# Kernel tuning notes

Measured on AMD Instinct MI355X. Metric: run time of the kernel, lower is better.

Reference implementation:

```python
import jax, jax.numpy as jnp
import numpy as np
import math

B, T, H = 2, 1024, 2048
NH, NKV, HD = 8, 2, 256
S = 4           # altup_num_inputs
FF = 8192       # intermediate_size
LR = 64         # laurel_rank
EPS = 1e-6
ROPE_THETA = 1e6


def _ln(x, w):
    # Gemma3nRMSNorm in this repo: fp32 mean-subtract then F.layer_norm (no bias)
    x32 = x.astype(jnp.float32)
    xc = x32 - x32.mean(-1, keepdims=True)
    var = (xc * xc).mean(-1, keepdims=True)
    return (xc * jax.lax.rsqrt(var + EPS) * w.astype(jnp.float32)).astype(x.dtype)


def _rotate_half(x):
    x1, x2 = jnp.split(x, 2, axis=-1)
    return jnp.concatenate((-x2, x1), axis=-1)


def _rope(x, cos, sin):  # x: [B,nh,T,hd]; cos/sin: [B,T,hd]
    return x * cos[:, None] + _rotate_half(x) * sin[:, None]


def setup_inputs() -> dict:
    key = jax.random.key(0)
    ks = jax.random.split(key, 24)

    def w(k, shape, scale=0.02):
        return jax.random.normal(k, shape, jnp.float32) * scale

    hidden_states = jax.random.normal(ks[0], (S, B, T, H), jnp.float32)

    # real rotary embeddings
    inv_freq = 1.0 / (ROPE_THETA ** (np.arange(0, HD, 2, dtype=np.float64) / HD))
    freqs = np.arange(T, dtype=np.float64)[:, None] * inv_freq[None, :]
    emb = np.concatenate([freqs, freqs], axis=-1)  # [T,HD]
    cos = jnp.broadcast_to(jnp.asarray(np.cos(emb), jnp.float32)[None], (B, T, HD))
    sin = jnp.broadcast_to(jnp.asarray(np.sin(emb), jnp.float32)[None], (B, T, HD))

    return {
        "hidden_states": hidden_states, "cos": cos, "sin": sin,
        "wq": w(ks[1], (NH * HD, H)), "wk": w(ks[2], (NKV * HD, H)),
        "wv": w(ks[3], (NKV * HD, H)), "wo": w(ks[4], (H, NH * HD)),
        "q_norm_w": jnp.ones((HD,), jnp.float32), "k_norm_w": jnp.ones((HD,), jnp.float32),
        "input_ln_w": jnp.ones((H,), jnp.float32), "post_attn_ln_w": jnp.ones((H,), jnp.float32),
        "pre_ffw_ln_w": jnp.ones((H,), jnp.float32), "post_ffw_ln_w": jnp.ones((H,), jnp.float32),
        "gate_w": w(ks[5], (FF, H)), "up_w": w(ks[6], (FF, H)), "down_w": w(ks[7], (H, FF)),
        "laurel_left_w": w(ks[8], (LR, H)), "laurel_right_w": w(ks[9], (H, LR)),
        "laurel_norm_w": jnp.ones((H,), jnp.float32),
        "router_norm_w": jnp.ones((H,), jnp.float32),
        "router_w": w(ks[10], (S, H)),
        "pred_coef_w": w(ks[11], (S * S, S)),
        "corr_coef_w": w(ks[12], (S, S)),
        "correct_output_scale": w(ks[13], (H,), 1.0),
    }


def reference(hidden_states, cos, sin, wq, wk, wv, wo, q_norm_w, k_norm_w,
              input_ln_w, post_attn_ln_w, pre_ffw_ln_w, post_ffw_ln_w,
              gate_w, up_w, down_w, laurel_left_w, laurel_right_w, laurel_norm_w,
              router_norm_w, router_w, pred_coef_w, corr_coef_w, correct_output_scale):
    def modalities_of(x):  # router: RMSNorm -> scale -> linear -> tanh
        r = _ln(x, router_norm_w) * (1.0 / H)
        return jnp.tanh((r @ router_w.T).astype(jnp.float32)).astype(x.dtype)

    # ---- AltUp predict ----
    m = modalities_of(hidden_states[0])                      # [B,T,S]
    coefs = (m @ pred_coef_w.T).reshape(B, T, S, S)          # raw [B,T,S_out,S_in]
    # torch: matmul(h.permute(1,2,3,0), coefs.permute(0,1,3,2)) => sum_s h[s]*raw[...,j,s]
    predictions = jnp.einsum('sbth,btjs->jbth', hidden_states, coefs) + hidden_states

    active = predictions[0]
    x_norm = _ln(active, input_ln_w)

    # ---- Laurel block ----
    lau = (x_norm @ laurel_left_w.T) @ laurel_right_w.T
    laurel_out = x_norm + _ln(lau, laurel_norm_w)

    # ---- Attention (GQA, q/k/v norms, rope, scale=1.0) ----
    q = _ln((x_norm @ wq.T).reshape(B, T, NH, HD), q_norm_w).transpose(0, 2, 1, 3)
    q = _rope(q, cos, sin)
    k = _ln((x_norm @ wk.T).reshape(B, T, NKV, HD), k_norm_w).transpose(0, 2, 1, 3)
    k = _rope(k, cos, sin)
    v = _ln((x_norm @ wv.T).reshape(B, T, NKV, HD), jnp.ones((HD,), jnp.float32))
    v = v.transpose(0, 2, 1, 3)
    rep = NH // NKV
    k = jnp.repeat(k, rep, axis=1)
    v = jnp.repeat(v, rep, axis=1)
    scores = jnp.einsum('bhqd,bhkd->bhqk', q, k)             # scaling = 1.0 in Gemma3n
    causal = jnp.tril(jnp.ones((T, T), bool))
    scores = jnp.where(causal, scores, jnp.finfo(jnp.float32).min)
    attn = jax.nn.softmax(scores.astype(jnp.float32), axis=-1).astype(q.dtype)
    out = jnp.einsum('bhqk,bhkd->bhqd', attn, v)
    out = out.transpose(0, 2, 1, 3).reshape(B, T, NH * HD) @ wo.T
    out = _ln(out, post_attn_ln_w)

    attn_gated = active + out
    attn_laurel = (attn_gated + laurel_out) * (1.0 / math.sqrt(2.0))

    # ---- MLP (gelu-tanh gated) ----
    h = _ln(attn_laurel, pre_ffw_ln_w)
    ffw = (jax.nn.gelu(h @ gate_w.T, approximate=True) * (h @ up_w.T)) @ down_w.T
    ffw = _ln(ffw, post_ffw_ln_w)
    activated = attn_laurel + ffw

    # ---- AltUp correct ----
    mc = modalities_of(activated)                            # [B,T,S]
    innovation = activated - predictions[0]                  # [B,T,H]
    ccoefs = (mc @ corr_coef_w.T) + 1.0                      # [B,T,S]
    corrected = innovation[None] * ccoefs.transpose(2, 0, 1)[..., None] + predictions

    # scale_corrected_output on the active stream (altup_correct_scale=True)
    first = (corrected[0] * correct_output_scale).astype(corrected.dtype)
    corrected = corrected.at[0].set(first)
    return corrected
```

## Files before the change

### kernel.cpp

```cpp
#include <hip/hip_runtime.h>
#include <hip/hip_bf16.h>
#include <math.h>

#define B_   2
#define T_   1024
#define H_   2048
#define NH_  8
#define NKV_ 2
#define HD_  256
#define S_   4
#define FF_  8192
#define LR_  64
#define ROWS_ (B_*T_)
#define EPS_ 1e-6f

typedef __attribute__((ext_vector_type(8))) __bf16 bf16x8;
typedef __attribute__((ext_vector_type(4))) float floatx4;
typedef __attribute__((ext_vector_type(8))) unsigned short ushort8v;

__device__ __forceinline__ unsigned short f2bf(float f) {
    unsigned int u = __float_as_uint(f);
    return (unsigned short)((u + 0x7FFFu + ((u >> 16) & 1u)) >> 16);
}

__device__ __forceinline__ float block_sum(float v) {
    __shared__ float s4[4];
    #pragma unroll
    for (int o = 32; o > 0; o >>= 1) v += __shfl_down(v, o, 64);
    int lane = threadIdx.x & 63;
    int w    = threadIdx.x >> 6;
    __syncthreads();
    if (lane == 0) s4[w] = v;
    __syncthreads();
    return s4[0] + s4[1] + s4[2] + s4[3];
}

__device__ __forceinline__ float block_max(float v) {
    __shared__ float s4m[4];
    #pragma unroll
    for (int o = 32; o > 0; o >>= 1) v = fmaxf(v, __shfl_down(v, o, 64));
    int lane = threadIdx.x & 63;
    int w    = threadIdx.x >> 6;
    __syncthreads();
    if (lane == 0) s4m[w] = v;
    __syncthreads();
    return fmaxf(fmaxf(s4m[0], s4m[1]), fmaxf(s4m[2], s4m[3]));
}

__global__ __launch_bounds__(256) void cvt_bf16(
    const float* __restrict__ in, unsigned short* __restrict__ out, int n)
{
    int i = (blockIdx.x * 256 + threadIdx.x) * 8;
    if (i >= n) return;
    float4 v0 = *reinterpret_cast<const float4*>(in + i);
    float4 v1 = *reinterpret_cast<const float4*>(in + i + 4);
    ushort8v o;
    o[0] = f2bf(v0.x); o[1] = f2bf(v0.y); o[2] = f2bf(v0.z); o[3] = f2bf(v0.w);
// ... 33 lines not shown
    const float* __restrict__ pcw, float* __restrict__ pred)
{
    size_t row = blockIdx.x;
    int tid = threadIdx.x;
    __shared__ float ms[4];
    __shared__ float c[16];
    if (tid < 4) ms[tid] = m[row * S_ + tid];
    __syncthreads();
    if (tid < 16) {
        float s = 0.f;
        #pragma unroll
        for (int i = 0; i < 4; ++i) s += ms[i] * pcw[tid * 4 + i];
        c[tid] = s;
    }
    __syncthreads();
    const size_t STRIDE = (size_t)ROWS_ * H_;
    #pragma unroll
    for (int i = 0; i < 8; ++i) {
        size_t idx = row * H_ + i*256 + tid;
        float h0 = hid[idx];
        float h1 = hid[idx + STRIDE];
        float h2 = hid[idx + 2*STRIDE];
        float h3 = hid[idx + 3*STRIDE];
        float hv[4] = {h0, h1, h2, h3};
        #pragma unroll
        for (int j = 0; j < 4; ++j) {
            float val = hv[j] + h0*c[j*4+0] + h1*c[j*4+1] + h2*c[j*4+2] + h3*c[j*4+3];
            pred[idx + (size_t)j * STRIDE] = val;
        }
    }
}

__global__ __launch_bounds__(256) void ln_residual(
    const float* __restrict__ x, const float* __restrict__ w,
    const float* __restrict__ a1, const float* __restrict__ a2,
    float scale, float* __restrict__ out, unsigned short* __restrict__ outb)
{
    size_t row = blockIdx.x;
    int tid = threadIdx.x;
    const float* xr = x + row * H_;
    float v[8]; float s = 0.f;
    #pragma unroll
    for (int i = 0; i < 8; ++i) { v[i] = xr[i*256 + tid]; s += v[i]; }
    float mu = block_sum(s) * (1.f / H_);
    float ss = 0.f;
    #pragma unroll
    for (int i = 0; i < 8; ++i) { float c = v[i] - mu; ss += c * c; }
    float rstd = rsqrtf(block_sum(ss) * (1.f / H_) + EPS_);
    #pragma unroll
    for (int i = 0; i < 8; ++i) {
        size_t idx = row * H_ + i*256 + tid;
        float y = (v[i] - mu) * rstd * w[i*256 + tid];
        if (a1) y += a1[idx];
        if (a2) y += a2[idx];
        y *= scale;
        if (out)  out[idx]  = y;
        if (outb) outb[idx] = f2bf(y);
    }
}

#define BM 64
#define BN 64
#define BK 32
#define LDP 68

__global__ __launch_bounds__(256) void gemm_nt(
    const float* __restrict__ A, const float* __restrict__ Bm,
    float* __restrict__ C, int M, int N, int K)
{
    __shared__ float As[BK][LDP];
    __shared__ float Bs[BK][LDP];
    int tid = threadIdx.x;
    int n0 = blockIdx.x * BN;
    int m0 = blockIdx.y * BM;
    int tx = tid & 15, ty = tid >> 4;
    int lrow = tid >> 3;
// ... 2 lines not shown
    for (int k0 = 0; k0 < K; k0 += BK) {
        #pragma unroll
        for (int r = 0; r < 2; ++r) {
            int row = lrow + r * 32;
            float4 a4 = *reinterpret_cast<const float4*>(&A[(size_t)(m0 + row) * K + k0 + lk]);
            As[lk+0][row] = a4.x; As[lk+1][row] = a4.y; As[lk+2][row] = a4.z; As[lk+3][row] = a4.w;
            float4 b4 = *reinterpret_cast<const float4*>(&Bm[(size_t)(n0 + row) * K + k0 + lk]);
            Bs[lk+0][row] = b4.x; Bs[lk+1][row] = b4.y; Bs[lk+2][row] = b4.z; Bs[lk+3][row] = b4.w;
        }
        __syncthreads();
        #pragma unroll
        for (int k = 0; k < BK; ++k) {
            float4 av = *reinterpret_cast<const float4*>(&As[k][ty << 2]);
            float4 bv = *reinterpret_cast<const float4*>(&Bs[k][tx << 2]);
            float a[4] = {av.x, av.y, av.z, av.w};
            float b[4] = {bv.x, bv.y, bv.z, bv.w};
            #pragma unroll
            for (int i = 0; i < 4; ++i)
                #pragma unroll
                for (int j = 0; j < 4; ++j)
                    acc[i][j] = fmaf(a[i], b[j], acc[i][j]);
        }
        __syncthreads();
    }
    #pragma unroll
    for (int i = 0; i < 4; ++i) {
        float4 o; o.x = acc[i][0]; o.y = acc[i][1]; o.z = acc[i][2]; o.w = acc[i][3];
        *reinterpret_cast<float4*>(&C[(size_t)(m0 + (ty << 2) + i) * N + n0 + (tx << 2)]) = o;
    }
}

__global__ __launch_bounds__(256) void gemm_bf16nt(
    const unsigned short* __restrict__ A, const unsigned short* __restrict__ Bm,
    float* __restrict__ C, int M, int N, int K)
{
    __shared__ unsigned short As[4096];
    __shared__ unsigned short Bs[4096];
    int tid = threadIdx.x;
    int lane = tid & 63;
    int wave = tid >> 6;
    int m0 = blockIdx.y * 128, n0 = blockIdx.x * 128;
    int wm = (wave >> 1) * 64;
    int wn = (wave & 1) * 64;
    floatx4 acc[4][4] = {};

    int cm = tid >> 2;
    int ck = tid & 3;
    const unsigned short* aP0 = A  + (size_t)(m0 + cm)      * K + ck * 8;
    const unsigned short* aP1 = A  + (size_t)(m0 + 64 + cm) * K + ck * 8;
    const unsigned short* bP0 = Bm + (size_t)(n0 + cm)      * K + ck * 8;
    const unsigned short* bP1 = Bm + (size_t)(n0 + 64 + cm) * K + ck * 8;
    unsigned short* aW0 = &As[(ck * 128 + cm) * 8];
    unsigned short* aW1 = &As[(ck * 128 + 64 + cm) * 8];
    unsigned short* bW0 = &Bs[(ck * 128 + cm) * 8];
    unsigned short* bW1 = &Bs[(ck * 128 + 64 + cm) * 8];

    uint4 ra0 = *reinterpret_cast<const uint4*>(aP0);
    uint4 ra1 = *reinterpret_cast<const uint4*>(aP1);
    uint4 rb0 = *reinterpret_cast<const uint4*>(bP0);
    uint4 rb1 = *reinterpret_cast<const uint4*>(bP1);

    int kc = lane >> 4, mr = lane & 15;
    for (int k0 = 0; k0 < K; k0 += 32) {
        __syncthreads();
        *reinterpret_cast<uint4*>(aW0) = ra0;
        *reinterpret_cast<uint4*>(aW1) = ra1;
        *reinterpret_cast<uint4*>(bW0) = rb0;
        *reinterpret_cast<uint4*>(bW1) = rb1;
        __syncthreads();
        if (k0 + 32 < K) {
            ra0 = *reinterpret_cast<const uint4*>(aP0 + k0 + 32);
            ra1 = *reinterpret_cast<const uint4*>(aP1 + k0 + 32);
            rb0 = *reinterpret_cast<const uint4*>(bP0 + k0 + 32);
            rb1 = *reinterpret_cast<const uint4*>(bP1 + k0 + 32);
        }
        bf16x8 af[4], bfv[4];
        #pragma unroll
        for (int mi = 0; mi < 4; ++mi)
            af[mi] = *reinterpret_cast<const bf16x8*>(&As[kc * 1024 + (wm + mi * 16 + mr) * 8]);
        #pragma unroll
        for (int ni = 0; ni < 4; ++ni)
            bfv[ni] = *reinterpret_cast<const bf16x8*>(&Bs[kc * 1024 + (wn + ni * 16 + mr) * 8]);
        #pragma unroll
        for (int mi = 0; mi < 4; ++mi)
            #pragma unroll
            for (int ni = 0; ni < 4; ++ni)
                acc[mi][ni] = __builtin_amdgcn_mfma_f32_16x16x32_bf16(af[mi], bfv[ni], acc[mi][ni], 0, 0, 0);
    }
    int quad = lane >> 4;
    #pragma unroll
    for (int mi = 0; mi < 4; ++mi)
        #pragma unroll
        for (int ni = 0; ni < 4; ++ni)
            #pragma unroll
            for (int r = 0; r < 4; ++r)
                C[(size_t)(m0 + wm + mi * 16 + quad * 4 + r) * N + n0 + wn + ni * 16 + mr] = acc[mi][ni][r];
}

__global__ __launch_bounds__(256) void gemm_gateup_bf16(
    const unsigned short* __restrict__ A, const unsigned short* __restrict__ G,
    const unsigned short* __restrict__ U, unsigned short* __restrict__ Cbf,
    int M, int N, int K)
{
    __shared__ unsigned short As[4096];
    __shared__ unsigned short Gs[2048];
    __shared__ unsigned short Us[2048];
    int tid = threadIdx.x;
    int lane = tid & 63;
    int wave = tid >> 6;
    int m0 = blockIdx.y * 128, n0 = blockIdx.x * 64;
    floatx4 accg[2][4] = {};
    floatx4 accu[2][4] = {};

    int cm = tid >> 2;
    int ck = tid & 3;
    const unsigned short* aP0 = A + (size_t)(m0 + cm)      * K + ck * 8;
    const unsigned short* aP1 = A + (size_t)(m0 + 64 + cm) * K + ck * 8;
    const unsigned short* gP  = G + (size_t)(n0 + cm)      * K + ck * 8;
    const unsigned short* uP  = U + (size_t)(n0 + cm)      * K + ck * 8;
    unsigned short* aW0 = &As[(ck * 128 + cm) * 8];
    unsigned short* aW1 = &As[(ck * 128 + 64 + cm) * 8];
    unsigned short* gW  = &Gs[(ck * 64 + cm) * 8];
    unsigned short* uW  = &Us[(ck * 64 + cm) * 8];

    uint4 ra0 = *reinterpret_cast<const uint4*>(aP0);
    uint4 ra1 = *reinterpret_cast<const uint4*>(aP1);
    uint4 rg  = *reinterpret_cast<const uint4*>(gP);
    uint4 ru  = *reinterpret_cast<const uint4*>(uP);

    int kc = lane >> 4, mr = lane & 15;
    for (int k0 = 0; k0 < K; k0 += 32) {
        __syncthreads();
        *reinterpret_cast<uint4*>(aW0) = ra0;
        *reinterpret_cast<uint4*>(aW1) = ra1;
        *reinterpret_cast<uint4*>(gW)  = rg;
        *reinterpret_cast<uint4*>(uW)  = ru;
        __syncthreads();
        if (k0 + 32 < K) {
            ra0 = *reinterpret_cast<const uint4*>(aP0 + k0 + 32);
            ra1 = *reinterpret_cast<const uint4*>(aP1 + k0 + 32);
            rg  = *reinterpret_cast<const uint4*>(gP + k0 + 32);
            ru  = *reinterpret_cast<const uint4*>(uP + k0 + 32);
        }
        bf16x8 af[2], gf[4], uf[4];
        #pragma unroll
        for (int mi = 0; mi < 2; ++mi)
            af[mi] = *reinterpret_cast<const bf16x8*>(&As[kc * 1024 + (wave * 32 + mi * 16 + mr) * 8]);
        #pragma unroll
        for (int ni = 0; ni < 4; ++ni) {
            gf[ni] = *reinterpret_cast<const bf16x8*>(&Gs[kc * 512 + (ni * 16 + mr) * 8]);
            uf[ni] = *reinterpret_cast<const bf16x8*>(&Us[kc * 512 + (ni * 16 + mr) * 8]);
        }
        #pragma unroll
        for (int mi = 0; mi < 2; ++mi)
            #pragma unroll
            for (int ni = 0; ni < 4; ++ni) {
                accg[mi][ni] = __builtin_amdgcn_mfma_f32_16x16x32_bf16(af[mi], gf[ni], accg[mi][ni], 0, 0, 0);
                accu[mi][ni] = __builtin_amdgcn_mfma_f32_16x16x32_bf16(af[mi], uf[ni], accu[mi][ni], 0, 0, 0);
            }
    }
    int quad = lane >> 4;
    #pragma unroll
    for (int mi = 0; mi < 2; ++mi) {
        int rb = m0 + wave * 32 + mi * 16 + quad * 4;
        #pragma unroll
        for (int ni = 0; ni < 4; ++ni)
            #pragma unroll
            for (int r = 0; r < 4; ++r) {
                float g = accg[mi][ni][r];
                float gl = 0.5f * g * (1.f + tanhf(0.7978845608028654f * (g + 0.044715f * g * g * g)));
                float val = gl * accu[mi][ni][r];
                Cbf[(size_t)(rb + r) * N + n0 + ni * 16 + mr] = f2bf(val);
            }
    }
}

__global__ __launch_bounds__(256) void qkv_norm_rope_bf(
    const float* __restrict__ in, const float* __restrict__ w,
    const float* __restrict__ cs, const float* __restrict__ sn,
    unsigned short* __restrict__ out, int nh, int do_rope, int transpose,
    int stride, int base)
{
    int blk = blockIdx.x;
    int h = blk % nh;
    int trow = blk / nh;
    int b = trow / T_;
    int t = trow % T_;
    int d = threadIdx.x;
    float x = in[(size_t)trow * stride + base + h * HD_ + d];
    float mu = block_sum(x) * (1.f / HD_);
    float xc = x - mu;
    float var = block_sum(xc * xc) * (1.f / HD_);
    float n = xc * rsqrtf(var + EPS_) * (w ? w[d] : 1.f);
    __shared__ float buf[HD_];
    buf[d] = n;
    __syncthreads();
    float val = n;
    if (do_rope) {
        float c = cs[(size_t)trow * HD_ + d];
        float s = sn[(size_t)trow * HD_ + d];
        float other = (d < 128) ? -buf[d + 128] : buf[d - 128];
        val = n * c + other * s;
    }
    size_t off;
    if (transpose)
        off = (((size_t)b * nh + h) * HD_ + d) * T_ + t;
    else
        off = (((size_t)b * nh + h) * T_ + t) * HD_ + d;
    out[off] = f2bf(val);
}

__global__ __launch_bounds__(256) void qk_gemm(
    const unsigned short* __restrict__ Q, const unsigned short* __restrict__ Kt,
    float* __restrict__ S, int head_base)
{
    if (blockIdx.x > blockIdx.y) return;
    const int K = HD_;
    const int N = T_;
    int z = blockIdx.z;
    const unsigned short* A  = Q  + (size_t)(head_base + z) * T_ * HD_;
    const unsigned short* Bm = Kt + (size_t)(head_base >> 2) * T_ * HD_;
    float* C = S + (size_t)z * T_ * T_;

    __shared__ unsigned short As[4096];
    __shared__ unsigned short Bs[4096];
    int tid = threadIdx.x;
    int lane = tid & 63;
    int wave = tid >> 6;
    int m0 = blockIdx.y * 128, n0 = blockIdx.x * 128;
    int wm = (wave >> 1) * 64;
    int wn = (wave & 1) * 64;
    floatx4 acc[4][4] = {};

    int cm = tid >> 2;
    int ck = tid & 3;
    const unsigned short* aP0 = A  + (size_t)(m0 + cm)      * K + ck * 8;
    const unsigned short* aP1 = A  + (size_t)(m0 + 64 + cm) * K + ck * 8;
    const unsigned short* bP0 = Bm + (size_t)(n0 + cm)      * K + ck * 8;
    const unsigned short* bP1 = Bm + (size_t)(n0 + 64 + cm) * K + ck * 8;
    unsigned short* aW0 = &As[(ck * 128 + cm) * 8];
    unsigned short* aW1 = &As[(ck * 128 + 64 + cm) * 8];
    unsigned short* bW0 = &Bs[(ck * 128 + cm) * 8];
    unsigned short* bW1 = &Bs[(ck * 128 + 64 + cm) * 8];

    uint4 ra0 = *reinterpret_cast<const uint4*>(aP0);
    uint4 ra1 = *reinterpret_cast<const uint4*>(aP1);
    uint4 rb0 = *reinterpret_cast<const uint4*>(bP0);
    uint4 rb1 = *reinterpret_cast<const uint4*>(bP1);

    int kc = lane >> 4, mr = lane & 15;
    for (int k0 = 0; k0 < K; k0 += 32) {
        __syncthreads();
        *reinterpret_cast<uint4*>(aW0) = ra0;
        *reinterpret_cast<uint4*>(aW1) = ra1;
        *reinterpret_cast<uint4*>(bW0) = rb0;
        *reinterpret_cast<uint4*>(bW1) = rb1;
        __syncthreads();
        if (k0 + 32 < K) {
            ra0 = *reinterpret_cast<const uint4*>(aP0 + k0 + 32);
            ra1 = *reinterpret_cast<const uint4*>(aP1 + k0 + 32);
            rb0 = *reinterpret_cast<const uint4*>(bP0 + k0 + 32);
            rb1 = *reinterpret_cast<const uint4*>(bP1 + k0 + 32);
        }
        bf16x8 af[4], bfv[4];
        #pragma unroll
        for (int mi = 0; mi < 4; ++mi)
            af[mi] = *reinterpret_cast<const bf16x8*>(&As[kc * 1024 + (wm + mi * 16 + mr) * 8]);
        #pragma unroll
        for (int ni = 0; ni < 4; ++ni)
            bfv[ni] = *reinterpret_cast<const bf16x8*>(&Bs[kc * 1024 + (wn + ni * 16 + mr) * 8]);
        #pragma unroll
        for (int mi = 0; mi < 4; ++mi)
            #pragma unroll
            for (int ni = 0; ni < 4; ++ni)
                acc[mi][ni] = __builtin_amdgcn_mfma_f32_16x16x32_bf16(af[mi], bfv[ni], acc[mi][ni], 0, 0, 0);
    }
    int quad = lane >> 4;
    #pragma unroll
    for (int mi = 0; mi < 4; ++mi)
        #pragma unroll
        for (int ni = 0; ni < 4; ++ni)
            #pragma unroll
            for (int r = 0; r < 4; ++r)
                C[(size_t)(m0 + wm + mi * 16 + quad * 4 + r) * N + n0 + wn + ni * 16 + mr] = acc[mi][ni][r];
}

__global__ __launch_bounds__(256) void softmax_causal(
    const float* __restrict__ S, unsigned short* __restrict__ P)
{
    int qi = blockIdx.x;
    int g  = blockIdx.y;
    int tid = threadIdx.x;
    int L = qi + 1;
    const float* Srow = S + ((size_t)g * T_ + qi) * T_;
    unsigned short* Prow = P + ((size_t)g * T_ + qi) * T_;
    float v[4];
    float mx = -3.402823466e38f;
    #pragma unroll
    for (int i = 0; i < 4; ++i) {
        int idx = i * 256 + tid;
        v[i] = (idx < L) ? Srow[idx] : -3.402823466e38f;
        mx = fmaxf(mx, v[i]);
    }
    mx = block_max(mx);
    float sm = 0.f;
    float e[4];
    #pragma unroll
    for (int i = 0; i < 4; ++i) {
        int idx = i * 256 + tid;
        e[i] = (idx < L) ? expf(v[i] - mx) : 0.f;
        sm += e[i];
    }
    sm = block_sum(sm);
    float inv = 1.f / sm;
    #pragma unroll
    for (int i = 0; i < 4; ++i)
        Prow[i * 256 + tid] = f2bf(e[i] * inv);
}

__global__ __launch_bounds__(256) void pv_gemm(
    const unsigned short* __restrict__ P, const unsigned short* __restrict__ Vt,
    unsigned short* __restrict__ Out, int head_base)
{
    const int K = T_;
    int z = blockIdx.z;
    int bh = head_base + z;
    int b = bh >> 3;
    int h = bh & 7;
    const unsigned short* A  = P  + (size_t)z * T_ * T_;
    const unsigned short* Bm = Vt + (size_t)(head_base >> 2) * HD_ * T_;

    __shared__ unsigned short As[4096];
    __shared__ unsigned short Bs[4096];
    int tid = threadIdx.x;
    int lane = tid & 63;
    int wave = tid >> 6;
    int m0 = blockIdx.y * 128, n0 = blockIdx.x * 128;
    int Kend = m0 + 128;
    int wm = (wave >> 1) * 64;
    int wn = (wave & 1) * 64;
    floatx4 acc[4][4] = {};

    int cm = tid >> 2;
    int ck = tid & 3;
    const unsigned short* aP0 = A  + (size_t)(m0 + cm)      * K + ck * 8;
    const unsigned short* aP1 = A  + (size_t)(m0 + 64 + cm) * K + ck * 8;
    const unsigned short* bP0 = Bm + (size_t)(n0 + cm)      * K + ck * 8;
    const unsigned short* bP1 = Bm + (size_t)(n0 + 64 + cm) * K + ck * 8;
    unsigned short* aW0 = &As[(ck * 128 + cm) * 8];
    unsigned short* aW1 = &As[(ck * 128 + 64 + cm) * 8];
    unsigned short* bW0 = &Bs[(ck * 128 + cm) * 8];
    unsigned short* bW1 = &Bs[(ck * 128 + 64 + cm) * 8];

    uint4 ra0 = *reinterpret_cast<const uint4*>(aP0);
    uint4 ra1 = *reinterpret_cast<const uint4*>(aP1);
    uint4 rb0 = *reinterpret_cast<const uint4*>(bP0);
    uint4 rb1 = *reinterpret_cast<const uint4*>(bP1);

    int kc = lane >> 4, mr = lane & 15;
    for (int k0 = 0; k0 < Kend; k0 += 32) {
        __syncthreads();
        *reinterpret_cast<uint4*>(aW0) = ra0;
        *reinterpret_cast<uint4*>(aW1) = ra1;
        *reinterpret_cast<uint4*>(bW0) = rb0;
        *reinterpret_cast<uint4*>(bW1) = rb1;
        __syncthreads();
        if (k0 + 32 < Kend) {
            ra0 = *reinterpret_cast<const uint4*>(aP0 + k0 + 32);
            ra1 = *reinterpret_cast<const uint4*>(aP1 + k0 + 32);
            rb0 = *reinterpret_cast<const uint4*>(bP0 + k0 + 32);
            rb1 = *reinterpret_cast<const uint4*>(bP1 + k0 + 32);
        }
        bf16x8 af[4], bfv[4];
        #pragma unroll
        for (int mi = 0; mi < 4; ++mi)
            af[mi] = *reinterpret_cast<const bf16x8*>(&As[kc * 1024 + (wm + mi * 16 + mr) * 8]);
        #pragma unroll
        for (int ni = 0; ni < 4; ++ni)
            bfv[ni] = *reinterpret_cast<const bf16x8*>(&Bs[kc * 1024 + (wn + ni * 16 + mr) * 8]);
        #pragma unroll
        for (int mi = 0; mi < 4; ++mi)
            #pragma unroll
            for (int ni = 0; ni < 4; ++ni)
                acc[mi][ni] = __builtin_amdgcn_mfma_f32_16x16x32_bf16(af[mi], bfv[ni], acc[mi][ni], 0, 0, 0);
    }
    int quad = lane >> 4;
    #pragma unroll
    for (int mi = 0; mi < 4; ++mi)
        #pragma unroll
        for (int ni = 0; ni < 4; ++ni)
            #pragma unroll
            for (int r = 0; r < 4; ++r) {
                int row = m0 + wm + mi * 16 + quad * 4 + r;
                int col = n0 + wn + ni * 16 + mr;
                Out[((size_t)(b * T_ + row)) * (NH_ * HD_) + h * HD_ + col] =
                    f2bf(acc[mi][ni][r]);
            }
}

__global__ __launch_bounds__(256) void correct_kernel(
    const float* __restrict__ act, const float* __restrict__ pred,
    const float* __restrict__ mc, const float* __restrict__ ccw,
    const float* __restrict__ cscale, float* __restrict__ out)
{
    size_t row = blockIdx.x;
// ... 39 lines not shown
    const float* wo             = (const float*)d_in[6];
    const float* q_norm_w       = (const float*)d_in[7];
    const float* k_norm_w       = (const float*)d_in[8];
    const float* input_ln_w     = (const float*)d_in[9];
    const float* post_attn_ln_w = (const float*)d_in[10];
    const float* pre_ffw_ln_w   = (const float*)d_in[11];
    const float* post_ffw_ln_w  = (const float*)d_in[12];
    const float* gate_w         = (const float*)d_in[13];
    const float* up_w           = (const float*)d_in[14];
    const float* down_w         = (const float*)d_in[15];
    const float* ll_w           = (const float*)d_in[16];
    const float* lr_w           = (const float*)d_in[17];
    const float* laurel_norm_w  = (const float*)d_in[18];
    const float* router_norm_w  = (const float*)d_in[19];
    const float* router_w       = (const float*)d_in[20];
    const float* pred_coef_w    = (const float*)d_in[21];
    const float* corr_coef_w    = (const float*)d_in[22];
    const float* cscale         = (const float*)d_in[23];
    float* outp = (float*)d_out;

    char* base = (char*)d_ws;
    float* pred   = (float*)base;              base += 67108864;
    float* xnorm  = (float*)base;              base += 16777216;
    unsigned short* xnorm_bf = (unsigned short*)base; base += 8388608;
    float* lout   = (float*)base;              base += 16777216;
    float* alaur  = (float*)base;              base += 16777216;
    float* tmpH   = (float*)base;              base += 16777216;
    float* mbuf   = (float*)base;              base += 32768;
    float* mcbuf  = (float*)base;              base += 32768;
    float* ltmp   = (float*)base;              base += 524288;
    char* arena = base;
    unsigned short* qkvw_bf = (unsigned short*)arena;
    float* qkv_pre = (float*)(arena + 12582912);
    unsigned short* q_bf    = (unsigned short*)(arena + 37748736);
    unsigned short* k_bf    = (unsigned short*)(arena + 46137344);
    unsigned short* vT_bf   = (unsigned short*)(arena + 48234496);
    unsigned short* attn_bf = (unsigned short*)(arena + 50331648);
    unsigned short* wo_bf   = (unsigned short*)(arena + 58720256);
    float* Sbuf             = (float*)(arena + 67108864);
    unsigned short* Pbuf    = (unsigned short*)(arena + 83886080);
    unsigned short* gate_bf = (unsigned short*)arena;
    unsigned short* up_bf   = (unsigned short*)(arena + 33554432);
    unsigned short* gu_bf   = (unsigned short*)(arena + 67108864);
    unsigned short* down_bf = gate_bf;
    float* activated = lout;

    router_kernel <<<ROWS_, 256, 0, stream>>>(hidden, router_norm_w, router_w, mbuf);
    predict_kernel<<<ROWS_, 256, 0, stream>>>(hidden, mbuf, pred_coef_w, pred);
    ln_residual   <<<ROWS_, 256, 0, stream>>>(pred, input_ln_w, nullptr, nullptr, 1.f, xnorm, xnorm_bf);

    gemm_nt<<<dim3(LR_/BN, ROWS_/BM), 256, 0, stream>>>(xnorm, ll_w, ltmp, ROWS_, LR_, H_);
    gemm_nt<<<dim3(H_/BN,  ROWS_/BM), 256, 0, stream>>>(ltmp, lr_w, tmpH, ROWS_, H_, LR_);
    ln_residual<<<ROWS_, 256, 0, stream>>>(tmpH, laurel_norm_w, xnorm, nullptr, 1.f, lout, nullptr);

    cvt_bf16<<<2048, 256, 0, stream>>>(wq, qkvw_bf,            4194304);
    cvt_bf16<<< 512, 256, 0, stream>>>(wk, qkvw_bf + 4194304,  1048576);
    cvt_bf16<<< 512, 256, 0, stream>>>(wv, qkvw_bf + 5242880,  1048576);
    gemm_bf16nt<<<dim3(24, 16), 256, 0, stream>>>(xnorm_bf, qkvw_bf, qkv_pre, ROWS_, 3072, H_);
    qkv_norm_rope_bf<<<ROWS_*NH_,  256, 0, stream>>>(qkv_pre, q_norm_w, cosp, sinp, q_bf,  NH_,  1, 0, 3072, 0);
    qkv_norm_rope_bf<<<ROWS_*NKV_, 256, 0, stream>>>(qkv_pre, k_norm_w, cosp, sinp, k_bf,  NKV_, 1, 0, 3072, 2048);
    qkv_norm_rope_bf<<<ROWS_*NKV_, 256, 0, stream>>>(qkv_pre, nullptr,  cosp, sinp, vT_bf, NKV_, 0, 1, 3072, 2560);
    for (int hb = 0; hb < B_ * NH_; hb += 4) {
        qk_gemm       <<<dim3(8, 8, 4), 256, 0, stream>>>(q_bf, k_bf, Sbuf, hb);
        softmax_causal<<<dim3(T_, 4),   256, 0, stream>>>(Sbuf, Pbuf);
        pv_gemm       <<<dim3(2, 8, 4), 256, 0, stream>>>(Pbuf, vT_bf, attn_bf, hb);
    }
    cvt_bf16<<<2048, 256, 0, stream>>>(wo, wo_bf, 4194304);
    gemm_bf16nt<<<dim3(16, 16), 256, 0, stream>>>(attn_bf, wo_bf, tmpH, ROWS_, H_, NH_*HD_);
    ln_residual<<<ROWS_, 256, 0, stream>>>(tmpH, post_attn_ln_w, pred, lout, 0.7071067811865475f, alaur, nullptr);

    ln_residual<<<ROWS_, 256, 0, stream>>>(alaur, pre_ffw_ln_w, nullptr, nullptr, 1.f, nullptr, xnorm_bf);
    cvt_bf16<<<8192, 256, 0, stream>>>(gate_w, gate_bf, 16777216);
    cvt_bf16<<<8192, 256, 0, stream>>>(up_w,   up_bf,   16777216);
    gemm_gateup_bf16<<<dim3(128, 16), 256, 0, stream>>>(xnorm_bf, gate_bf, up_bf, gu_bf, ROWS_, FF_, H_);
    cvt_bf16<<<8192, 256, 0, stream>>>(down_w, down_bf, 16777216);
    gemm_bf16nt<<<dim3(16, 16), 256, 0, stream>>>(gu_bf, down_bf, tmpH, ROWS_, H_, FF_);
    ln_residual<<<ROWS_, 256, 0, stream>>>(tmpH, post_ffw_ln_w, alaur, nullptr, 1.f, activated, nullptr);

    router_kernel <<<ROWS_, 256, 0, stream>>>(activated, router_norm_w, router_w, mcbuf);
    correct_kernel<<<ROWS_, 256, 0, stream>>>(activated, pred, mcbuf, corr_coef_w, cscale, outp);
}
```

Baseline: 1.180 ms.

## Use direct global-to-LDS loads, split-K GEMMs, fused QKV norm, batched attention

Replaces the register-staged prefetch in all MFMA GEMMs with global_load_lds direct-to-LDS copies. Adds a two-way split-K to the output and down projections, writing partial sums to a scratch buffer that the following layernorm adds in. Fuses the three q/k/v norm-rope launches into one kernel and batches attention over 8 heads per launch, with a single PV GEMM over all heads. The intent is to raise occupancy and parallelism and cut launch count. In exchange it loses the register prefetch overlap, adds extra partial-sum traffic, and reuses the xnorm buffer as scratch after its earlier consumers.

Result: no change. 1.202 ms (+1.9%).

```diff
diff --git a/kernel.cpp b/kernel.cpp
--- a/kernel.cpp
+++ b/kernel.cpp
@@ -23,6 +23,12 @@
     return (unsigned short)((u + 0x7FFFu + ((u >> 16) & 1u)) >> 16);
 }
 
+__device__ __forceinline__ void gl_lds16(const void* g, void* l) {
+    __builtin_amdgcn_global_load_lds(
+        (const __attribute__((address_space(1))) void*)g,
+        (__attribute__((address_space(3))) void*)l, 16, 0, 0);
+}
+
 __device__ __forceinline__ float block_sum(float v) {
     __shared__ float s4[4];
     #pragma unroll
@@ -122,16 +128,22 @@
 }
 
 __global__ __launch_bounds__(256) void ln_residual(
-    const float* __restrict__ x, const float* __restrict__ w,
+    const float* __restrict__ x, const float* __restrict__ xadd,
+    const float* __restrict__ w,
     const float* __restrict__ a1, const float* __restrict__ a2,
     float scale, float* __restrict__ out, unsigned short* __restrict__ outb)
 {
     size_t row = blockIdx.x;
     int tid = threadIdx.x;
     const float* xr = x + row * H_;
+    const float* xa = xadd ? xadd + row * H_ : nullptr;
     float v[8]; float s = 0.f;
     #pragma unroll
-    for (int i = 0; i < 8; ++i) { v[i] = xr[i*256 + tid]; s += v[i]; }
+    for (int i = 0; i < 8; ++i) {
+        v[i] = xr[i*256 + tid];
+        if (xa) v[i] += xa[i*256 + tid];
+        s += v[i];
+    }
     float mu = block_sum(s) * (1.f / H_);
     float ss = 0.f;
     #pragma unroll
@@ -200,8 +212,175 @@
 
 __global__ __launch_bounds__(256) void gemm_bf16nt(
     const unsigned short* __restrict__ A, const unsigned short* __restrict__ Bm,
-    float* __restrict__ C, int M, int N, int K)
-{
+    float* __restrict__ C, float* __restrict__ C2, int M, int N, int K)
+{
+    __shared__ unsigned short As[4096];
+    __shared__ unsigned short Bs[4096];
+    int tid = threadIdx.x;
+    int lane = tid & 63;
+    int wave = tid >> 6;
+    int m0 = blockIdx.y * 128, n0 = blockIdx.x * 128;
+    int Kper = K / gridDim.z;
+    int kbeg = blockIdx.z * Kper;
+    int kend = kbeg + Kper;
+    int wm = (wave >> 1) * 64;
+    int wn = (wave & 1) * 64;
+    floatx4 acc[4][4] = {};
+
+    const unsigned short* aG0 = A  + (size_t)(m0 + lane)      * K + wave * 8;
+    const unsigned short* aG1 = A  + (size_t)(m0 + 64 + lane) * K + wave * 8;
+    const unsigned short* bG0 = Bm + (size_t)(n0 + lane)      * K + wave * 8;
+    const unsigned short* bG1 = Bm + (size_t)(n0 + 64 + lane) * K + wave * 8;
+    unsigned short* aL0 = &As[wave * 1024];
+    unsigned short* aL1 = &As[wave * 1024 + 512];
+    unsigned short* bL0 = &Bs[wave * 1024];
+    unsigned short* bL1 = &Bs[wave * 1024 + 512];
+
+    int kc = lane >> 4, mr = lane & 15;
+    for (int k0 = kbeg; k0 < kend; k0 += 32) {
+        __syncthreads();
+        gl_lds16(aG0 + k0, aL0);
+        gl_lds16(aG1 + k0, aL1);
+        gl_lds16(bG0 + k0, bL0);
+        gl_lds16(bG1 + k0, bL1);
+        __syncthreads();
+        bf16x8 af[4], bfv[4];
+        #pragma unroll
+        for (int mi = 0; mi < 4; ++mi)
+            af[mi] = *reinterpret_cast<const bf16x8*>(&As[kc * 1024 + (wm + mi * 16 + mr) * 8]);
+        #pragma unroll
+        for (int ni = 0; ni < 4; ++ni)
+            bfv[ni] = *reinterpret_cast<const bf16x8*>(&Bs[kc * 1024 + (wn + ni * 16 + mr) * 8]);
+        #pragma unroll
+        for (int mi = 0; mi < 4; ++mi)
+            #pragma unroll
+            for (int ni = 0; ni < 4; ++ni)
+                acc[mi][ni] = __builtin_amdgcn_mfma_f32_16x16x32_bf16(af[mi], bfv[ni], acc[mi][ni], 0, 0, 0);
+    }
+    float* Cout = (blockIdx.z == 0) ? C : C2;
+    int quad = lane >> 4;
+    #pragma unroll
+    for (int mi = 0; mi < 4; ++mi)
+        #pragma unroll
+        for (int ni = 0; ni < 4; ++ni)
+            #pragma unroll
+            for (int r = 0; r < 4; ++r)
+                Cout[(size_t)(m0 + wm + mi * 16 + quad * 4 + r) * N + n0 + wn + ni * 16 + mr] = acc[mi][ni][r];
+}
+
+__global__ __launch_bounds__(256) void gemm_gateup_bf16(
+    const unsigned short* __restrict__ A, const unsigned short* __restrict__ G,
+    const unsigned short* __restrict__ U, unsigned short* __restrict__ Cbf,
+    int M, int N, int K)
+{
+    __shared__ unsigned short As[4096];
+    __shared__ unsigned short Gs[2048];
+    __shared__ unsigned short Us[2048];
+    int tid = threadIdx.x;
+    int lane = tid & 63;
+    int wave = tid >> 6;
+    int m0 = blockIdx.y * 128, n0 = blockIdx.x * 64;
+    floatx4 accg[2][4] = {};
+    floatx4 accu[2][4] = {};
+
+    const unsigned short* aG0 = A + (size_t)(m0 + lane)      * K + wave * 8;
+    const unsigned short* aG1 = A + (size_t)(m0 + 64 + lane) * K + wave * 8;
+    const unsigned short* gG  = G + (size_t)(n0 + lane)      * K + wave * 8;
+    const unsigned short* uG  = U + (size_t)(n0 + lane)      * K + wave * 8;
+    unsigned short* aL0 = &As[wave * 1024];
+    unsigned short* aL1 = &As[wave * 1024 + 512];
+    unsigned short* gL  = &Gs[wave * 512];
+    unsigned short* uL  = &Us[wave * 512];
+
+    int kc = lane >> 4, mr = lane & 15;
+    for (int k0 = 0; k0 < K; k0 += 32) {
+        __syncthreads();
+        gl_lds16(aG0 + k0, aL0);
+        gl_lds16(aG1 + k0, aL1);
+        gl_lds16(gG + k0, gL);
+        gl_lds16(uG + k0, uL);
+        __syncthreads();
+        bf16x8 af[2], gf[4], uf[4];
+        #pragma unroll
+        for (int mi = 0; mi < 2; ++mi)
+            af[mi] = *reinterpret_cast<const bf16x8*>(&As[kc * 1024 + (wave * 32 + mi * 16 + mr) * 8]);
+        #pragma unroll
+        for (int ni = 0; ni < 4; ++ni) {
+            gf[ni] = *reinterpret_cast<const bf16x8*>(&Gs[kc * 512 + (ni * 16 + mr) * 8]);
+            uf[ni] = *reinterpret_cast<const bf16x8*>(&Us[kc * 512 + (ni * 16 + mr) * 8]);
+        }
+        #pragma unroll
+        for (int mi = 0; mi < 2; ++mi)
+            #pragma unroll
+            for (int ni = 0; ni < 4; ++ni) {
+                accg[mi][ni] = __builtin_amdgcn_mfma_f32_16x16x32_bf16(af[mi], gf[ni], accg[mi][ni], 0, 0, 0);
+                accu[mi][ni] = __builtin_amdgcn_mfma_f32_16x16x32_bf16(af[mi], uf[ni], accu[mi][ni], 0, 0, 0);
+            }
+    }
+    int quad = lane >> 4;
+    #pragma unroll
+    for (int mi = 0; mi < 2; ++mi) {
+        int rb = m0 + wave * 32 + mi * 16 + quad * 4;
+        #pragma unroll
+        for (int ni = 0; ni < 4; ++ni)
+            #pragma unroll
+            for (int r = 0; r < 4; ++r) {
+                float g = accg[mi][ni][r];
+                float gl = 0.5f * g * (1.f + tanhf(0.7978845608028654f * (g + 0.044715f * g * g * g)));
+                float val = gl * accu[mi][ni][r];
+                Cbf[(size_t)(rb + r) * N + n0 + ni * 16 + mr] = f2bf(val);
+            }
+    }
+}
+
+__global__ __launch_bounds__(256) void qkv_norm_rope_fused(
+    const float* __restrict__ in, const float* __restrict__ qw,
+    const float* __restrict__ kw,
+    const float* __restrict__ cs, const float* __restrict__ sn,
+    unsigned short* __restrict__ qo, unsigned short* __restrict__ ko,
+    unsigned short* __restrict__ vo)
+{
+    int blk = blockIdx.x;
+    int hh = blk % 12;
+    int trow = blk / 12;
+    int b = trow / T_;
+    int t = trow % T_;
+    int d = threadIdx.x;
+    float x = in[(size_t)trow * 3072 + hh * HD_ + d];
+    float mu = block_sum(x) * (1.f / HD_);
+    float xc = x - mu;
+    float var = block_sum(xc * xc) * (1.f / HD_);
+    float wv_ = (hh < 8) ? qw[d] : (hh < 10 ? kw[d] : 1.f);
+    float n = xc * rsqrtf(var + EPS_) * wv_;
+    __shared__ float buf[HD_];
+    buf[d] = n;
+    __syncthreads();
+    float val = n;
+    if (hh < 10) {
+        float c = cs[(size_t)trow * HD_ + d];
+        float s = sn[(size_t)trow * HD_ + d];
+        float other = (d < 128) ? -buf[d + 128] : buf[d - 128];
+        val = n * c + other * s;
+    }
+    if (hh < 8)
+        qo[(((size_t)b * NH_ + hh) * T_ + t) * HD_ + d] = f2bf(val);
+    else if (hh < 10)
+        ko[(((size_t)b * NKV_ + (hh - 8)) * T_ + t) * HD_ + d] = f2bf(val);
+    else
+        vo[(((size_t)b * NKV_ + (hh - 10)) * HD_ + d) * T_ + t] = f2bf(val);
+}
+
+__global__ __launch_bounds__(256) void qk_gemm(
+    const unsigned short* __restrict__ Q, const unsigned short* __restrict__ Kt,
+    float* __restrict__ S, int head_base)
+{
+    if (blockIdx.x > blockIdx.y) return;
+    int z = blockIdx.z;
+    int bh = head_base + z;
+    const unsigned short* A  = Q  + (size_t)bh * T_ * HD_;
+    const unsigned short* Bm = Kt + (size_t)(bh >> 2) * T_ * HD_;
+    float* C = S + (size_t)z * T_ * T_;
+
     __shared__ unsigned short As[4096];
     __shared__ unsigned short Bs[4096];
     int tid = threadIdx.x;
@@ -212,36 +391,23 @@
     int wn = (wave & 1) * 64;
     floatx4 acc[4][4] = {};
 
-    int cm = tid >> 2;
-    int ck = tid & 3;
-    const unsigned short* aP0 = A  + (size_t)(m0 + cm)      * K + ck * 8;
-    const unsigned short* aP1 = A  + (size_t)(m0 + 64 + cm) * K + ck * 8;
-    const unsigned short* bP0 = Bm + (size_t)(n0 + cm)      * K + ck * 8;
-    const unsigned short* bP1 = Bm + (size_t)(n0 + 64 + cm) * K + ck * 8;
-    unsigned short* aW0 = &As[(ck * 128 + cm) * 8];
-    unsigned short* aW1 = &As[(ck * 128 + 64 + cm) * 8];
-    unsigned short* bW0 = &Bs[(ck * 128 + cm) * 8];
-    unsigned short* bW1 = &Bs[(ck * 128 + 64 + cm) * 8];
-
-    uint4 ra0 = *reinterpret_cast<const uint4*>(aP0);
-    uint4 ra1 = *reinterpret_cast<const uint4*>(aP1);
-    uint4 rb0 = *reinterpret_cast<const uint4*>(bP0);
-    uint4 rb1 = *reinterpret_cast<const uint4*>(bP1);
+    const unsigned short* aG0 = A  + (size_t)(m0 + lane)      * HD_ + wave * 8;
+    const unsigned short* aG1 = A  + (size_t)(m0 + 64 + lane) * HD_ + wave * 8;
+    const unsigned short* bG0 = Bm + (size_t)(n0 + lane)      * HD_ + wave * 8;
+    const unsigned short* bG1 = Bm + (size_t)(n0 + 64 + lane) * HD_ + wave * 8;
+    unsigned short* aL0 = &As[wave * 1024];
+    unsigned short* aL1 = &As[wave * 1024 + 512];
+    unsigned short* bL0 = &Bs[wave * 1024];
+    unsigned short* bL1 = &Bs[wave * 1024 + 512];
 
     int kc = lane >> 4, mr = lane & 15;
-    for (int k0 = 0; k0 < K; k0 += 32) {
-        __syncthreads();
-        *reinterpret_cast<uint4*>(aW0) = ra0;
-        *reinterpret_cast<uint4*>(aW1) = ra1;
-        *reinterpret_cast<uint4*>(bW0) = rb0;
-        *reinterpret_cast<uint4*>(bW1) = rb1;
-        __syncthreads();
-        if (k0 + 32 < K) {
-            ra0 = *reinterpret_cast<const uint4*>(aP0 + k0 + 32);
-            ra1 = *reinterpret_cast<const uint4*>(aP1 + k0 + 32);
-            rb0 = *reinterpret_cast<const uint4*>(bP0 + k0 + 32);
-            rb1 = *reinterpret_cast<const uint4*>(bP1 + k0 + 32);
-        }
+    for (int k0 = 0; k0 < HD_; k0 += 32) {
+        __syncthreads();
+        gl_lds16(aG0 + k0, aL0);
+        gl_lds16(aG1 + k0, aL1);
+        gl_lds16(bG0 + k0, bL0);
+        gl_lds16(bG1 + k0, bL1);
+        __syncthreads();
         bf16x8 af[4], bfv[4];
         #pragma unroll
         for (int mi = 0; mi < 4; ++mi)
@@ -262,195 +428,7 @@
         for (int ni = 0; ni < 4; ++ni)
             #pragma unroll
             for (int r = 0; r < 4; ++r)
-                C[(size_t)(m0 + wm + mi * 16 + quad * 4 + r) * N + n0 + wn + ni * 16 + mr] = acc[mi][ni][r];
-}
-
-__global__ __launch_bounds__(256) void gemm_gateup_bf16(
-    const unsigned short* __restrict__ A, const unsigned short* __restrict__ G,
-    const unsigned short* __restrict__ U, unsigned short* __restrict__ Cbf,
-    int M, int N, int K)
-{
-    __shared__ unsigned short As[4096];
-    __shared__ unsigned short Gs[2048];
-    __shared__ unsigned short Us[2048];
-    int tid = threadIdx.x;
-    int lane = tid & 63;
-    int wave = tid >> 6;
-    int m0 = blockIdx.y * 128, n0 = blockIdx.x * 64;
-    floatx4 accg[2][4] = {};
-    floatx4 accu[2][4] = {};
-
-    int cm = tid >> 2;
-    int ck = tid & 3;
-    const unsigned short* aP0 = A + (size_t)(m0 + cm)      * K + ck * 8;
-    const unsigned short* aP1 = A + (size_t)(m0 + 64 + cm) * K + ck * 8;
-    const unsigned short* gP  = G + (size_t)(n0 + cm)      * K + ck * 8;
-    const unsigned short* uP  = U + (size_t)(n0 + cm)      * K + ck * 8;
-    unsigned short* aW0 = &As[(ck * 128 + cm) * 8];
-    unsigned short* aW1 = &As[(ck * 128 + 64 + cm) * 8];
-    unsigned short* gW  = &Gs[(ck * 64 + cm) * 8];
-    unsigned short* uW  = &Us[(ck * 64 + cm) * 8];
-
-    uint4 ra0 = *reinterpret_cast<const uint4*>(aP0);
-    uint4 ra1 = *reinterpret_cast<const uint4*>(aP1);
-    uint4 rg  = *reinterpret_cast<const uint4*>(gP);
-    uint4 ru  = *reinterpret_cast<const uint4*>(uP);
-
-    int kc = lane >> 4, mr = lane & 15;
-    for (int k0 = 0; k0 < K; k0 += 32) {
-        __syncthreads();
-        *reinterpret_cast<uint4*>(aW0) = ra0;
-        *reinterpret_cast<uint4*>(aW1) = ra1;
-        *reinterpret_cast<uint4*>(gW)  = rg;
-        *reinterpret_cast<uint4*>(uW)  = ru;
-        __syncthreads();
-        if (k0 + 32 < K) {
-            ra0 = *reinterpret_cast<const uint4*>(aP0 + k0 + 32);
-            ra1 = *reinterpret_cast<const uint4*>(aP1 + k0 + 32);
-            rg  = *reinterpret_cast<const uint4*>(gP + k0 + 32);
-            ru  = *reinterpret_cast<const uint4*>(uP + k0 + 32);
-        }
-        bf16x8 af[2], gf[4], uf[4];
-        #pragma unroll
-        for (int mi = 0; mi < 2; ++mi)
-            af[mi] = *reinterpret_cast<const bf16x8*>(&As[kc * 1024 + (wave * 32 + mi * 16 + mr) * 8]);
-        #pragma unroll
-        for (int ni = 0; ni < 4; ++ni) {
-            gf[ni] = *reinterpret_cast<const bf16x8*>(&Gs[kc * 512 + (ni * 16 + mr) * 8]);
-            uf[ni] = *reinterpret_cast<const bf16x8*>(&Us[kc * 512 + (ni * 16 + mr) * 8]);
-        }
-        #pragma unroll
-        for (int mi = 0; mi < 2; ++mi)
-            #pragma unroll
-            for (int ni = 0; ni < 4; ++ni) {
-                accg[mi][ni] = __builtin_amdgcn_mfma_f32_16x16x32_bf16(af[mi], gf[ni], accg[mi][ni], 0, 0, 0);
-                accu[mi][ni] = __builtin_amdgcn_mfma_f32_16x16x32_bf16(af[mi], uf[ni], accu[mi][ni], 0, 0, 0);
-            }
-    }
-    int quad = lane >> 4;
-    #pragma unroll
-    for (int mi = 0; mi < 2; ++mi) {
-        int rb = m0 + wave * 32 + mi * 16 + quad * 4;
-        #pragma unroll
-        for (int ni = 0; ni < 4; ++ni)
-            #pragma unroll
-            for (int r = 0; r < 4; ++r) {
-                float g = accg[mi][ni][r];
-                float gl = 0.5f * g * (1.f + tanhf(0.7978845608028654f * (g + 0.044715f * g * g * g)));
-                float val = gl * accu[mi][ni][r];
-                Cbf[(size_t)(rb + r) * N + n0 + ni * 16 + mr] = f2bf(val);
-            }
-    }
-}
-
-__global__ __launch_bounds__(256) void qkv_norm_rope_bf(
-    const float* __restrict__ in, const float* __restrict__ w,
-    const float* __restrict__ cs, const float* __restrict__ sn,
-    unsigned short* __restrict__ out, int nh, int do_rope, int transpose,
-    int stride, int base)
-{
-    int blk = blockIdx.x;
-    int h = blk % nh;
-    int trow = blk / nh;
-    int b = trow / T_;
-    int t = trow % T_;
-    int d = threadIdx.x;
-    float x = in[(size_t)trow * stride + base + h * HD_ + d];
-    float mu = block_sum(x) * (1.f / HD_);
-    float xc = x - mu;
-    float var = block_sum(xc * xc) * (1.f / HD_);
-    float n = xc * rsqrtf(var + EPS_) * (w ? w[d] : 1.f);
-    __shared__ float buf[HD_];
-    buf[d] = n;
-    __syncthreads();
-    float val = n;
-    if (do_rope) {
-        float c = cs[(size_t)trow * HD_ + d];
-        float s = sn[(size_t)trow * HD_ + d];
-        float other = (d < 128) ? -buf[d + 128] : buf[d - 128];
-        val = n * c + other * s;
-    }
-    size_t off;
-    if (transpose)
-        off = (((size_t)b * nh + h) * HD_ + d) * T_ + t;
-    else
-        off = (((size_t)b * nh + h) * T_ + t) * HD_ + d;
-    out[off] = f2bf(val);
-}
-
-__global__ __launch_bounds__(256) void qk_gemm(
-    const unsigned short* __restrict__ Q, const unsigned short* __restrict__ Kt,
-    float* __restrict__ S, int head_base)
-{
-    if (blockIdx.x > blockIdx.y) return;
-    const int K = HD_;
-    const int N = T_;
-    int z = blockIdx.z;
-    const unsigned short* A  = Q  + (size_t)(head_base + z) * T_ * HD_;
-    const unsigned short* Bm = Kt + (size_t)(head_base >> 2) * T_ * HD_;
-    float* C = S + (size_t)z * T_ * T_;
-
-    __shared__ unsigned short As[4096];
-    __shared__ unsigned short Bs[4096];
-    int tid = threadIdx.x;
-    int lane = tid & 63;
-    int wave = tid >> 6;
-    int m0 = blockIdx.y * 128, n0 = blockIdx.x * 128;
-    int wm = (wave >> 1) * 64;
-    int wn = (wave & 1) * 64;
-    floatx4 acc[4][4] = {};
-
-    int cm = tid >> 2;
-    int ck = tid & 3;
-    const unsigned short* aP0 = A  + (size_t)(m0 + cm)      * K + ck * 8;
-    const unsigned short* aP1 = A  + (size_t)(m0 + 64 + cm) * K + ck * 8;
-    const unsigned short* bP0 = Bm + (size_t)(n0 + cm)      * K + ck * 8;
-    const unsigned short* bP1 = Bm + (size_t)(n0 + 64 + cm) * K + ck * 8;
-    unsigned short* aW0 = &As[(ck * 128 + cm) * 8];
-    unsigned short* aW1 = &As[(ck * 128 + 64 + cm) * 8];
-    unsigned short* bW0 = &Bs[(ck * 128 + cm) * 8];
-    unsigned short* bW1 = &Bs[(ck * 128 + 64 + cm) * 8];
-
-    uint4 ra0 = *reinterpret_cast<const uint4*>(aP0);
-    uint4 ra1 = *reinterpret_cast<const uint4*>(aP1);
-    uint4 rb0 = *reinterpret_cast<const uint4*>(bP0);
-    uint4 rb1 = *reinterpret_cast<const uint4*>(bP1);
-
-    int kc = lane >> 4, mr = lane & 15;
-    for (int k0 = 0; k0 < K; k0 += 32) {
-        __syncthreads();
-        *reinterpret_cast<uint4*>(aW0) = ra0;
-        *reinterpret_cast<uint4*>(aW1) = ra1;
-        *reinterpret_cast<uint4*>(bW0) = rb0;
-        *reinterpret_cast<uint4*>(bW1) = rb1;
-        __syncthreads();
-        if (k0 + 32 < K) {
-            ra0 = *reinterpret_cast<const uint4*>(aP0 + k0 + 32);
-            ra1 = *reinterpret_cast<const uint4*>(aP1 + k0 + 32);
-            rb0 = *reinterpret_cast<const uint4*>(bP0 + k0 + 32);
-            rb1 = *reinterpret_cast<const uint4*>(bP1 + k0 + 32);
-        }
-        bf16x8 af[4], bfv[4];
-        #pragma unroll
-        for (int mi = 0; mi < 4; ++mi)
-            af[mi] = *reinterpret_cast<const bf16x8*>(&As[kc * 1024 + (wm + mi * 16 + mr) * 8]);
-        #pragma unroll
-        for (int ni = 0; ni < 4; ++ni)
-            bfv[ni] = *reinterpret_cast<const bf16x8*>(&Bs[kc * 1024 + (wn + ni * 16 + mr) * 8]);
-        #pragma unroll
-        for (int mi = 0; mi < 4; ++mi)
-            #pragma unroll
-            for (int ni = 0; ni < 4; ++ni)
-                acc[mi][ni] = __builtin_amdgcn_mfma_f32_16x16x32_bf16(af[mi], bfv[ni], acc[mi][ni], 0, 0, 0);
-    }
-    int quad = lane >> 4;
-    #pragma unroll
-    for (int mi = 0; mi < 4; ++mi)
-        #pragma unroll
-        for (int ni = 0; ni < 4; ++ni)
-            #pragma unroll
-            for (int r = 0; r < 4; ++r)
-                C[(size_t)(m0 + wm + mi * 16 + quad * 4 + r) * N + n0 + wn + ni * 16 + mr] = acc[mi][ni][r];
+                C[(size_t)(m0 + wm + mi * 16 + quad * 4 + r) * T_ + n0 + wn + ni * 16 + mr] = acc[mi][ni][r];
 }
 
 __global__ __launch_bounds__(256) void softmax_causal(
@@ -488,15 +466,13 @@
 
 __global__ __launch_bounds__(256) void pv_gemm(
     const unsigned short* __restrict__ P, const unsigned short* __restrict__ Vt,
-    unsigned short* __restrict__ Out, int head_base)
-{
-    const int K = T_;
+    unsigned short* __restrict__ Out)
+{
     int z = blockIdx.z;
-    int bh = head_base + z;
-    int b = bh >> 3;
-    int h = bh & 7;
+    int b = z >> 3;
+    int h = z & 7;
     const unsigned short* A  = P  + (size_t)z * T_ * T_;
-    const unsigned short* Bm = Vt + (size_t)(head_base >> 2) * HD_ * T_;
+    const unsigned short* Bm = Vt + (size_t)(z >> 2) * HD_ * T_;
 
     __shared__ unsigned short As[4096];
     __shared__ unsigned short Bs[4096];
@@ -509,36 +485,23 @@
     int wn = (wave & 1) * 64;
     floatx4 acc[4][4] = {};
 
-    int cm = tid >> 2;
-    int ck = tid & 3;
-    const unsigned short* aP0 = A  + (size_t)(m0 + cm)      * K + ck * 8;
-    const unsigned short* aP1 = A  + (size_t)(m0 + 64 + cm) * K + ck * 8;
-    const unsigned short* bP0 = Bm + (size_t)(n0 + cm)      * K + ck * 8;
-    const unsigned short* bP1 = Bm + (size_t)(n0 + 64 + cm) * K + ck * 8;
-    unsigned short* aW0 = &As[(ck * 128 + cm) * 8];
-    unsigned short* aW1 = &As[(ck * 128 + 64 + cm) * 8];
-    unsigned short* bW0 = &Bs[(ck * 128 + cm) * 8];
-    unsigned short* bW1 = &Bs[(ck * 128 + 64 + cm) * 8];
-
-    uint4 ra0 = *reinterpret_cast<const uint4*>(aP0);
-    uint4 ra1 = *reinterpret_cast<const uint4*>(aP1);
-    uint4 rb0 = *reinterpret_cast<const uint4*>(bP0);
-    uint4 rb1 = *reinterpret_cast<const uint4*>(bP1);
+    const unsigned short* aG0 = A  + (size_t)(m0 + lane)      * T_ + wave * 8;
+    const unsigned short* aG1 = A  + (size_t)(m0 + 64 + lane) * T_ + wave * 8;
+    const unsigned short* bG0 = Bm + (size_t)(n0 + lane)      * T_ + wave * 8;
+    const unsigned short* bG1 = Bm + (size_t)(n0 + 64 + lane) * T_ + wave * 8;
+    unsigned short* aL0 = &As[wave * 1024];
+    unsigned short* aL1 = &As[wave * 1024 + 512];
+    unsigned short* bL0 = &Bs[wave * 1024];
+    unsigned short* bL1 = &Bs[wave * 1024 + 512];
 
     int kc = lane >> 4, mr = lane & 15;
     for (int k0 = 0; k0 < Kend; k0 += 32) {
         __syncthreads();
-        *reinterpret_cast<uint4*>(aW0) = ra0;
-        *reinterpret_cast<uint4*>(aW1) = ra1;
-        *reinterpret_cast<uint4*>(bW0) = rb0;
-        *reinterpret_cast<uint4*>(bW1) = rb1;
-        __syncthreads();
-        if (k0 + 32 < Kend) {
-            ra0 = *reinterpret_cast<const uint4*>(aP0 + k0 + 32);
-            ra1 = *reinterpret_cast<const uint4*>(aP1 + k0 + 32);
-            rb0 = *reinterpret_cast<const uint4*>(bP0 + k0 + 32);
-            rb1 = *reinterpret_cast<const uint4*>(bP1 + k0 + 32);
-        }
+        gl_lds16(aG0 + k0, aL0);
+        gl_lds16(aG1 + k0, aL1);
+        gl_lds16(bG0 + k0, bL0);
+        gl_lds16(bG1 + k0, bL1);
+        __syncthreads();
         bf16x8 af[4], bfv[4];
         #pragma unroll
         for (int mi = 0; mi < 4; ++mi)
@@ -644,13 +607,13 @@
     char* arena = base;
     unsigned short* qkvw_bf = (unsigned short*)arena;
     float* qkv_pre = (float*)(arena + 12582912);
+    unsigned short* Pbuf    = (unsigned short*)arena;
     unsigned short* q_bf    = (unsigned short*)(arena + 37748736);
     unsigned short* k_bf    = (unsigned short*)(arena + 46137344);
     unsigned short* vT_bf   = (unsigned short*)(arena + 48234496);
     unsigned short* attn_bf = (unsigned short*)(arena + 50331648);
     unsigned short* wo_bf   = (unsigned short*)(arena + 58720256);
     float* Sbuf             = (float*)(arena + 67108864);
-    unsigned short* Pbuf    = (unsigned short*)(arena + 83886080);
     unsigned short* gate_bf = (unsigned short*)arena;
     unsigned short* up_bf   = (unsigned short*)(arena + 33554432);
     unsigned short* gu_bf   = (unsigned short*)(arena + 67108864);
@@ -659,35 +622,33 @@
 
     router_kernel <<<ROWS_, 256, 0, stream>>>(hidden, router_norm_w, router_w, mbuf);
     predict_kernel<<<ROWS_, 256, 0, stream>>>(hidden, mbuf, pred_coef_w, pred);
-    ln_residual   <<<ROWS_, 256, 0, stream>>>(pred, input_ln_w, nullptr, nullptr, 1.f, xnorm, xnorm_bf);
+    ln_residual   <<<ROWS_, 256, 0, stream>>>(pred, nullptr, input_ln_w, nullptr, nullptr, 1.f, xnorm, xnorm_bf);
 
     gemm_nt<<<dim3(LR_/BN, ROWS_/BM), 256, 0, stream>>>(xnorm, ll_w, ltmp, ROWS_, LR_, H_);
     gemm_nt<<<dim3(H_/BN,  ROWS_/BM), 256, 0, stream>>>(ltmp, lr_w, tmpH, ROWS_, H_, LR_);
-    ln_residual<<<ROWS_, 256, 0, stream>>>(tmpH, laurel_norm_w, xnorm, nullptr, 1.f, lout, nullptr);
+    ln_residual<<<ROWS_, 256, 0, stream>>>(tmpH, nullptr, laurel_norm_w, xnorm, nullptr, 1.f, lout, nullptr);
 
     cvt_bf16<<<2048, 256, 0, stream>>>(wq, qkvw_bf,            4194304);
     cvt_bf16<<< 512, 256, 0, stream>>>(wk, qkvw_bf + 4194304,  1048576);
     cvt_bf16<<< 512, 256, 0, stream>>>(wv, qkvw_bf + 5242880,  1048576);
-    gemm_bf16nt<<<dim3(24, 16), 256, 0, stream>>>(xnorm_bf, qkvw_bf, qkv_pre, ROWS_, 3072, H_);
-    qkv_norm_rope_bf<<<ROWS_*NH_,  256, 0, stream>>>(qkv_pre, q_norm_w, cosp, sinp, q_bf,  NH_,  1, 0, 3072, 0);
-    qkv_norm_rope_bf<<<ROWS_*NKV_, 256, 0, stream>>>(qkv_pre, k_norm_w, cosp, sinp, k_bf,  NKV_, 1, 0, 3072, 2048);
-    qkv_norm_rope_bf<<<ROWS_*NKV_, 256, 0, stream>>>(qkv_pre, nullptr,  cosp, sinp, vT_bf, NKV_, 0, 1, 3072, 2560);
-    for (int hb = 0; hb < B_ * NH_; hb += 4) {
-        qk_gemm       <<<dim3(8, 8, 4), 256, 0, stream>>>(q_bf, k_bf, Sbuf, hb);
-        softmax_causal<<<dim3(T_, 4),   256, 0, stream>>>(Sbuf, Pbuf);
-        pv_gemm       <<<dim3(2, 8, 4), 256, 0, stream>>>(Pbuf, vT_bf, attn_bf, hb);
-    }
+    gemm_bf16nt<<<dim3(24, 16, 1), 256, 0, stream>>>(xnorm_bf, qkvw_bf, qkv_pre, nullptr, ROWS_, 3072, H_);
+    qkv_norm_rope_fused<<<ROWS_*12, 256, 0, stream>>>(qkv_pre, q_norm_w, k_norm_w, cosp, sinp, q_bf, k_bf, vT_bf);
     cvt_bf16<<<2048, 256, 0, stream>>>(wo, wo_bf, 4194304);
-    gemm_bf16nt<<<dim3(16, 16), 256, 0, stream>>>(attn_bf, wo_bf, tmpH, ROWS_, H_, NH_*HD_);
-    ln_residual<<<ROWS_, 256, 0, stream>>>(tmpH, post_attn_ln_w, pred, lout, 0.7071067811865475f, alaur, nullptr);
-
-    ln_residual<<<ROWS_, 256, 0, stream>>>(alaur, pre_ffw_ln_w, nullptr, nullptr, 1.f, nullptr, xnorm_bf);
+    for (int hb = 0; hb < B_ * NH_; hb += 8) {
+        qk_gemm       <<<dim3(8, 8, 8), 256, 0, stream>>>(q_bf, k_bf, Sbuf, hb);
+        softmax_causal<<<dim3(T_, 8),   256, 0, stream>>>(Sbuf, Pbuf + (size_t)hb * T_ * T_);
+    }
+    pv_gemm<<<dim3(2, 8, 16), 256, 0, stream>>>(Pbuf, vT_bf, attn_bf);
+    gemm_bf16nt<<<dim3(16, 16, 2), 256, 0, stream>>>(attn_bf, wo_bf, tmpH, xnorm, ROWS_, H_, NH_*HD_);
+    ln_residual<<<ROWS_, 256, 0, stream>>>(tmpH, xnorm, post_attn_ln_w, pred, lout, 0.7071067811865475f, alaur, nullptr);
+
+    ln_residual<<<ROWS_, 256, 0, stream>>>(alaur, nullptr, pre_ffw_ln_w, nullptr, nullptr, 1.f, nullptr, xnorm_bf);
     cvt_bf16<<<8192, 256, 0, stream>>>(gate_w, gate_bf, 16777216);
     cvt_bf16<<<8192, 256, 0, stream>>>(up_w,   up_bf,   16777216);
     gemm_gateup_bf16<<<dim3(128, 16), 256, 0, stream>>>(xnorm_bf, gate_bf, up_bf, gu_bf, ROWS_, FF_, H_);
     cvt_bf16<<<8192, 256, 0, stream>>>(down_w, down_bf, 16777216);
-    gemm_bf16nt<<<dim3(16, 16), 256, 0, stream>>>(gu_bf, down_bf, tmpH, ROWS_, H_, FF_);
-    ln_residual<<<ROWS_, 256, 0, stream>>>(tmpH, post_ffw_ln_w, alaur, nullptr, 1.f, activated, nullptr);
+    gemm_bf16nt<<<dim3(16, 16, 2), 256, 0, stream>>>(gu_bf, down_bf, tmpH, xnorm, ROWS_, H_, FF_);
+    ln_residual<<<ROWS_, 256, 0, stream>>>(tmpH, xnorm, post_ffw_ln_w, alaur, nullptr, 1.f, activated, nullptr);
 
     router_kernel <<<ROWS_, 256, 0, stream>>>(activated, router_norm_w, router_w, mcbuf);
     correct_kernel<<<ROWS_, 256, 0, stream>>>(activated, pred, mcbuf, corr_coef_w, cscale, outp);
```
